# Kernel tuning notes

Measured on AMD Instinct MI355X. Metric: run time of the kernel, lower is better.

The kernel has to match this reference:

```python
import jax, jax.numpy as jnp
import numpy as np

INP = 256
OUP = 256
FGROUP = 16
CGROUP = 8
K = 3
STRIDE = 1
PAD = K // 2
B, H, W = 16, 64, 64
O1 = OUP * INP * K * K // CGROUP  # 73728, glgf output channels


def setup_inputs() -> dict:
    key = jax.random.key(0)
    ks = jax.random.split(key, 11)
    s = 0.1  # keep sigmoid pre-activations in a sane range
    return {
        "x": jax.random.normal(ks[0], (B, INP, H, W), jnp.float32),
        # GLGF generating the dynamic conv weights (oup*inp*k*k//cgroup outputs)
        "g1_fc1_l": jax.random.normal(ks[1], (INP, INP // FGROUP), jnp.float32) * s,
        "g1_fc1_g1": jax.random.normal(ks[2], (FGROUP, INP // FGROUP), jnp.float32) * s,
        "g1_fc1_g2": jax.random.normal(ks[3], (INP, FGROUP), jnp.float32) * s,
        "g1_fc2_l": jax.random.normal(ks[4], (O1,), jnp.float32) * s,
        "g1_fc2_g": jax.random.normal(ks[5], (INP,), jnp.float32) * s,
        # GLGF generating the per-channel output gate c (oup outputs)
        "g2_fc1_l": jax.random.normal(ks[6], (INP, INP // FGROUP), jnp.float32) * s,
        "g2_fc1_g1": jax.random.normal(ks[7], (FGROUP, INP // FGROUP), jnp.float32) * s,
        "g2_fc1_g2": jax.random.normal(ks[8], (INP, FGROUP), jnp.float32) * s,
        "g2_fc2_l": jax.random.normal(ks[9], (OUP,), jnp.float32) * s,
        "g2_fc2_g": jax.random.normal(ks[10], (INP,), jnp.float32) * s,
    }


def glgf(g, w1l, w1g1, w1g2, w2l, w2g):
    """GLGF applied to a [B, inp] gap vector (all convs are 1x1 -> grouped linears)."""
    b, inp = g.shape
    gp = inp // FGROUP
    gg = g.reshape(b, FGROUP, gp)
    # wn_fc1_l: grouped (fgroup) inp->inp; weight [inp, inp//fgroup]
    local = jnp.einsum('bgi,goi->bgo', gg, w1l.reshape(FGROUP, gp, gp)).reshape(b, inp)
    # wn_fc1_g2(wn_fc1_g1(x)): inp->fgroup (grouped) then fgroup->inp (dense)
    glob = jnp.einsum('bgi,gi->bg', gg, w1g1) @ w1g2.T  # [b, inp]
    h = jax.nn.sigmoid(local + glob)
    # wn_fc2_l: groups=inp, inp->O; weight [O] (1 input channel per output)
    O = w2l.shape[0]
    local2 = (h[:, :, None] * w2l.reshape(inp, O // inp)).reshape(b, O)
    # wn_fc2_g: dense inp->1, broadcast-added
    glob2 = h @ w2g  # [b]
    return local2 + glob2[:, None]


def reference(x, g1_fc1_l, g1_fc1_g1, g1_fc1_g2, g1_fc2_l, g1_fc2_g,
              g2_fc1_l, g2_fc1_g1, g2_fc1_g2, g2_fc2_l, g2_fc2_g):
    b = x.shape[0]
    gap = x.mean(axis=(2, 3))  # adaptive_avg_pool2d to 1x1 -> [b, inp]
    # generate per-sample grouped conv weights: [b, oup, inp//cgroup, k, k]
    xw = glgf(gap, g1_fc1_l, g1_fc1_g1, g1_fc1_g2, g1_fc2_l, g1_fc2_g)
    w = xw.reshape(b, OUP, INP // CGROUP, K, K)
    # torch's groups=b*cgroup batch-trick == per-sample conv with groups=cgroup
    def conv_one(xi, wi):
        return jax.lax.conv_general_dilated(
            xi[None], wi, (STRIDE, STRIDE), [(PAD, PAD), (PAD, PAD)],
            feature_group_count=CGROUP,
            dimension_numbers=('NCHW', 'OIHW', 'NCHW'))[0]
    y = jax.vmap(conv_one)(x, w)  # [b, oup, H, W]
    # per-sample, per-channel gate
    c = glgf(gap, g2_fc1_l, g2_fc1_g1, g2_fc1_g2, g2_fc2_l, g2_fc2_g)  # [b, oup]
    return y * c[:, :, None, None]
```

## Files before the change

kernel.cpp:

```cpp
#include <hip/hip_runtime.h>
#include <cstddef>
#include <cstdint>

typedef __attribute__((ext_vector_type(8))) short bf16x8;
typedef __attribute__((ext_vector_type(4))) unsigned short ushort4v;
typedef __attribute__((ext_vector_type(8))) unsigned short ushort8v;
typedef __attribute__((ext_vector_type(16))) float f32x16;

__device__ __forceinline__ unsigned short f2bf(float f) {
  union { float f; unsigned u; } v; v.f = f;
  unsigned r = v.u + 0x7FFFu + ((v.u >> 16) & 1u);
  return (unsigned short)(r >> 16);
}

__device__ __forceinline__ void gload16(const void* g, void* l) {
  __builtin_amdgcn_global_load_lds(
      (const __attribute__((address_space(1))) void*)(unsigned long long)(uintptr_t)g,
      (__attribute__((address_space(3))) void*)(unsigned)(uintptr_t)l, 16, 0, 0);
}

#define PADC 132
__global__ __launch_bounds__(256) void prep_kernel(
    const float* __restrict__ x, unsigned short* __restrict__ xt,
    float* __restrict__ partials) {
  __shared__ unsigned short cm[32 * PADC];
  __shared__ float sred[32][32];
  const int bid = blockIdx.x;
  const int wkr = ((bid & 7) << 9) | (bid >> 3);
  const int yp = wkr & 31, g = (wkr >> 5) & 7, b = wkr >> 8;
  const int y0 = yp * 2;
  const int tid = threadIdx.x;
  const float* xg = x + (size_t)(b * 256 + g * 32) * 4096;

  float csum[4];
#pragma unroll
  for (int j = 0; j < 4; ++j) {
    const int idx = tid + 256 * j;
    const int ic = idx >> 5;
    const int r = idx & 31;
    const int ry = r >> 4, gx4 = (r & 15) * 4;
    const float4 v = *reinterpret_cast<const float4*>(
        xg + (size_t)ic * 4096 + (y0 + ry) * 64 + gx4);
    csum[j] = v.x + v.y + v.z + v.w;
    ushort4v s;
    s[0] = f2bf(v.x); s[1] = f2bf(v.y); s[2] = f2bf(v.z); s[3] = f2bf(v.w);
    *reinterpret_cast<ushort4v*>(&cm[ic * PADC + ry * 64 + gx4]) = s;
  }
#pragma unroll
  for (int j = 0; j < 4; ++j) {
    const int ic = (tid >> 5) + 8 * j;
    sred[ic][tid & 31] = csum[j];
  }
  __syncthreads();

  if (tid < 32) {
    float s = 0.f;
#pragma unroll
    for (int i = 0; i < 32; ++i) s += sred[tid][i];
    partials[(size_t)(b * 256 + g * 32 + tid) * 32 + yp] = s;
  }

  const size_t xtb = (size_t)(b * 8 + g) * (66 * 66 * 32);
#pragma unroll
  for (int jj = 0; jj < 2; ++jj) {
    const int o = tid + 256 * jj;
    const int px = o >> 2, icq = o & 3;
    const int ry = px >> 6, gx = px & 63;
    ushort8v t;
#pragma unroll
    for (int c2 = 0; c2 < 8; ++c2) t[c2] = cm[(icq * 8 + c2) * PADC + px];
    *reinterpret_cast<ushort8v*>(
        &xt[xtb + ((size_t)(y0 + ry + 1) * 66 + (gx + 1)) * 32 + icq * 8]) = t;
  }

  const ushort8v z = {0, 0, 0, 0, 0, 0, 0, 0};
  if (tid < 16) {
    const int rr = tid >> 3;
    const int side = (tid >> 2) & 1;
    const int icq = tid & 3;
    const int col = side * 65;
    *reinterpret_cast<ushort8v*>(
        &xt[xtb + ((size_t)(y0 + rr + 1) * 66 + col) * 32 + icq * 8]) = z;
  }
  if (yp == 0 || yp == 31) {
    const int row = (yp == 0) ? 0 : 65;
    for (int o = tid; o < 66 * 4; o += 256) {
      const int col = o >> 2, icq = o & 3;
      *reinterpret_cast<ushort8v*>(
          &xt[xtb + ((size_t)row * 66 + col) * 32 + icq * 8]) = z;
    }
  }
}

__global__ __launch_bounds__(256) void glgf_pack(
    const float* __restrict__ partials,
    const float* __restrict__ w1l, const float* __restrict__ w1g1,
    const float* __restrict__ w1g2, const float* __restrict__ w2l,
    const float* __restrict__ w2g,
    const float* __restrict__ v1l, const float* __restrict__ v1g1,
    const float* __restrict__ v1g2, const float* __restrict__ v2l,
    const float* __restrict__ v2g,
    unsigned short* __restrict__ wpack) {
  __shared__ float gapL[256];
  __shared__ float t1L[16];
  __shared__ float h1L[256];
  __shared__ float red[256];
  __shared__ float cLs[32];
  const int bid = blockIdx.x;
  const int bg = ((bid & 7) << 4) | (bid >> 3);
  const int g = bg & 7, b = bg >> 3;
  const int c = threadIdx.x;
  {
    float s = 0.f;
    const float* pp = partials + (size_t)(b * 256 + c) * 32;
#pragma unroll
    for (int i = 0; i < 32; ++i) s += pp[i];
    gapL[c] = s * (1.f / 4096.f);
  }
  __syncthreads();

  const int gbase = c & ~15;
  float local1 = 0.f;
#pragma unroll
  for (int i = 0; i < 16; ++i) local1 += gapL[gbase + i] * w1l[c * 16 + i];
  if (c < 16) {
    float t = 0.f;
#pragma unroll
    for (int i = 0; i < 16; ++i) t += gapL[c * 16 + i] * w1g1[c * 16 + i];
    t1L[c] = t;
  }
  __syncthreads();
  float glob1 = 0.f;
#pragma unroll
  for (int gg = 0; gg < 16; ++gg) glob1 += t1L[gg] * w1g2[c * 16 + gg];
  const float h1 = 1.f / (1.f + expf(-(local1 + glob1)));
  h1L[c] = h1;
  red[c] = h1 * w2g[c];
  __syncthreads();
  for (int s = 128; s > 0; s >>= 1) {
    if (c < s) red[c] += red[c + s];
    __syncthreads();
  }
  const float glob2 = red[0];

  float local2 = 0.f;
#pragma unroll
  for (int i = 0; i < 16; ++i) local2 += gapL[gbase + i] * v1l[c * 16 + i];
  if (c < 16) {
    float t = 0.f;
#pragma unroll
    for (int i = 0; i < 16; ++i) t += gapL[c * 16 + i] * v1g1[c * 16 + i];
    t1L[c] = t;
  }
  __syncthreads();
  float glob1b = 0.f;
#pragma unroll
  for (int gg = 0; gg < 16; ++gg) glob1b += t1L[gg] * v1g2[c * 16 + gg];
  const float h2 = 1.f / (1.f + expf(-(local2 + glob1b)));
  red[c] = h2 * v2g[c];
  __syncthreads();
  for (int s = 128; s > 0; s >>= 1) {
    if (c < s) red[c] += red[c + s];
    __syncthreads();
  }
  if (c < 32) {
    const int o = g * 32 + c;
    float l = 0.f;
#pragma unroll
    for (int i = 0; i < 16; ++i) l += gapL[(o & ~15) + i] * v1l[o * 16 + i];
    float gl = 0.f;
#pragma unroll
    for (int gg = 0; gg < 16; ++gg) gl += t1L[gg] * v1g2[o * 16 + gg];
    const float h2o = 1.f / (1.f + expf(-(l + gl)));
    cLs[c] = h2o * v2l[o] + red[0];
  }
  __syncthreads();

  unsigned short* wpo = wpack + (size_t)bg * 9216;
#pragma unroll 4
  for (int it = 0; it < 36; ++it) {
    const int idx = it * 256 + c;
    const int kk = idx >> 9;
    const int rem = idx & 511;
    const int l = rem >> 3, e = rem & 7;
    const int oc = l & 31, hi = l >> 5;
    const int ic = ((kk & 1) << 4) + hi * 8 + e;
    const int sp = kk >> 1;
    const int o = (g << 5) + oc;
    const float wv = h1L[o] * w2l[o * 288 + ic * 9 + sp] + glob2;
    wpo[idx] = f2bf(wv * cLs[oc]);
  }
}

__global__ __launch_bounds__(512, 4) void conv_kernel(
    const unsigned short* __restrict__ wpack,
    const unsigned short* __restrict__ xt, float* __restrict__ out) {
  __shared__ __align__(16) unsigned short wpl[9216];
  __shared__ __align__(16) unsigned short btile[21120];

  const int bid = blockIdx.x;
  const int wkr = ((bid & 7) << 7) | (bid >> 3);
  const int yq = wkr & 7;
  const int bg = wkr >> 3;
  const int g = bg & 7, b = bg >> 3;
  const int tid = threadIdx.x;
  const int lane = tid & 63, wave = tid >> 6;
  const int n = lane & 31, hi = lane >> 5;

  const char* xbase = (const char*)xt + (size_t)bg * 278784;
  const int y0 = yq * 8;

#pragma unroll
  for (int i = 0; i < 6; ++i) {
    const int li = i * 512 + tid;
    if (li < 2640) {
      const int r = li / 264, rem = li - r * 264;
      const int cqs = rem / 66, px = rem % 66;
      const int cq = cqs ^ (px & 3);
      gload16(xbase + (y0 + r) * 4224 + px * 64 + cq * 16,
              (char*)btile + i * 8192 + wave * 1024);
    }
  }

  {
    const uint4* src = reinterpret_cast<const uint4*>(wpack + (size_t)bg * 9216);
    uint4* dst = reinterpret_cast<uint4*>(wpl);
#pragma unroll
    for (int i = 0; i < 3; ++i) {
      const int li = i * 512 + tid;
      if (li < 1152) dst[li] = src[li];
    }
  }

  asm volatile("s_waitcnt vmcnt(0) lgkmcnt(0)\n\ts_barrier" ::: "memory");
  __builtin_amdgcn_sched_barrier(0);

  f32x16 acc0, acc1;
#pragma unroll
  for (int i = 0; i < 16; ++i) { acc0[i] = 0.f; acc1[i] = 0.f; }

  __builtin_amdgcn_s_setprio(1);
#pragma unroll
  for (int kk = 0; kk < 18; ++kk) {
    const int sp = kk >> 1;
    const int ky = sp / 3, kx = sp % 3;
    const int cq = ((kk & 1) << 1) + hi;
    const int pxA = n + kx;
    const int pxB = 32 + n + kx;
    const bf16x8 af =
        *reinterpret_cast<const bf16x8*>(&wpl[kk * 512 + lane * 8]);
    const bf16x8 bf0 = *reinterpret_cast<const bf16x8*>(
        &btile[((((wave + ky) << 2) + (cq ^ (pxA & 3))) * 66 + pxA) * 8]);
    const bf16x8 bf1 = *reinterpret_cast<const bf16x8*>(
        &btile[((((wave + ky) << 2) + (cq ^ (pxB & 3))) * 66 + pxB) * 8]);
    acc0 = __builtin_amdgcn_mfma_f32_32x32x16_bf16(af, bf0, acc0, 0, 0, 0);
    acc1 = __builtin_amdgcn_mfma_f32_32x32x16_bf16(af, bf1, acc1, 0, 0, 0);
  }
  __builtin_amdgcn_s_setprio(0);

  const int y = y0 + wave;
  float* ob = out + (size_t)(b * 256 + g * 32) * 4096 + y * 64 + n +
              (size_t)(hi << 2) * 4096;
#pragma unroll
  for (int r = 0; r < 16; ++r) {
    const int row = (r & 3) + ((r >> 2) << 3);
    ob[(size_t)row * 4096] = acc0[r];
    ob[(size_t)row * 4096 + 32] = acc1[r];
  }
}

extern "C" void kernel_launch(void* const* d_in, const int* in_sizes, int n_in,
                              void* d_out, int out_size, void* d_ws,
                              size_t ws_size, hipStream_t stream) {
  const float* x    = (const float*)d_in[0];
  const float* w1l  = (const float*)d_in[1];
  const float* w1g1 = (const float*)d_in[2];
  const float* w1g2 = (const float*)d_in[3];
  const float* w2l  = (const float*)d_in[4];
  const float* w2g  = (const float*)d_in[5];
  const float* v1l  = (const float*)d_in[6];
  const float* v1g1 = (const float*)d_in[7];
  const float* v1g2 = (const float*)d_in[8];
  const float* v2l  = (const float*)d_in[9];
  const float* v2g  = (const float*)d_in[10];
  float* out = (float*)d_out;

  unsigned short* xt = (unsigned short*)d_ws;
  float* partials = (float*)(xt + 17842176);
  unsigned short* wpack = (unsigned short*)(partials + 131072);

  prep_kernel<<<4096, 256, 0, stream>>>(x, xt, partials);
  glgf_pack<<<128, 256, 0, stream>>>(partials, w1l, w1g1, w1g2, w2l, w2g,
                                     v1l, v1g1, v1g2, v2l, v2g, wpack);
  conv_kernel<<<1024, 512, 0, stream>>>(wpack, xt, out);
}
```

Baseline: 52.58 us.

## Fuse bf16 transpose/padding into conv kernel, drop intermediate xt buffer

Removes the prep kernel that wrote a padded channel-last bf16 copy of x to workspace. A lean GAP reduction kernel now computes the pooled vector, and the conv kernel reads fp32 x directly, converts it to bf16 and writes the swizzled LDS tile with zero halos. This avoids writing and re-reading the roughly 35 MB intermediate. In exchange, the conv blocks re-read halo rows of x, issue strided scalar global loads (one per channel per lane), and give up the async global-to-LDS loads.

```diff
diff --git a/kernel.cpp b/kernel.cpp
--- a/kernel.cpp
+++ b/kernel.cpp
@@ -3,7 +3,6 @@
 #include <cstdint>
 
 typedef __attribute__((ext_vector_type(8))) short bf16x8;
-typedef __attribute__((ext_vector_type(4))) unsigned short ushort4v;
 typedef __attribute__((ext_vector_type(8))) unsigned short ushort8v;
 typedef __attribute__((ext_vector_type(16))) float f32x16;
 
@@ -13,87 +12,27 @@
   return (unsigned short)(r >> 16);
 }
 
-__device__ __forceinline__ void gload16(const void* g, void* l) {
-  __builtin_amdgcn_global_load_lds(
-      (const __attribute__((address_space(1))) void*)(unsigned long long)(uintptr_t)g,
-      (__attribute__((address_space(3))) void*)(unsigned)(uintptr_t)l, 16, 0, 0);
-}
-
-#define PADC 132
-__global__ __launch_bounds__(256) void prep_kernel(
-    const float* __restrict__ x, unsigned short* __restrict__ xt,
-    float* __restrict__ partials) {
-  __shared__ unsigned short cm[32 * PADC];
-  __shared__ float sred[32][32];
+__global__ __launch_bounds__(256) void gap_kernel(const float* __restrict__ x,
+                                                  float* __restrict__ gap) {
   const int bid = blockIdx.x;
-  const int wkr = ((bid & 7) << 9) | (bid >> 3);
-  const int yp = wkr & 31, g = (wkr >> 5) & 7, b = wkr >> 8;
-  const int y0 = yp * 2;
-  const int tid = threadIdx.x;
-  const float* xg = x + (size_t)(b * 256 + g * 32) * 4096;
-
-  float csum[4];
+  const float* p = x + (size_t)bid * 4096;
+  const int t = threadIdx.x;
+  float s = 0.f;
 #pragma unroll
   for (int j = 0; j < 4; ++j) {
-    const int idx = tid + 256 * j;
-    const int ic = idx >> 5;
-    const int r = idx & 31;
-    const int ry = r >> 4, gx4 = (r & 15) * 4;
-    const float4 v = *reinterpret_cast<const float4*>(
-        xg + (size_t)ic * 4096 + (y0 + ry) * 64 + gx4);
-    csum[j] = v.x + v.y + v.z + v.w;
-    ushort4v s;
-    s[0] = f2bf(v.x); s[1] = f2bf(v.y); s[2] = f2bf(v.z); s[3] = f2bf(v.w);
-    *reinterpret_cast<ushort4v*>(&cm[ic * PADC + ry * 64 + gx4]) = s;
-  }
-#pragma unroll
-  for (int j = 0; j < 4; ++j) {
-    const int ic = (tid >> 5) + 8 * j;
-    sred[ic][tid & 31] = csum[j];
-  }
-  __syncthreads();
-
-  if (tid < 32) {
-    float s = 0.f;
-#pragma unroll
-    for (int i = 0; i < 32; ++i) s += sred[tid][i];
-    partials[(size_t)(b * 256 + g * 32 + tid) * 32 + yp] = s;
-  }
-
-  const size_t xtb = (size_t)(b * 8 + g) * (66 * 66 * 32);
-#pragma unroll
-  for (int jj = 0; jj < 2; ++jj) {
-    const int o = tid + 256 * jj;
-    const int px = o >> 2, icq = o & 3;
-    const int ry = px >> 6, gx = px & 63;
-    ushort8v t;
-#pragma unroll
-    for (int c2 = 0; c2 < 8; ++c2) t[c2] = cm[(icq * 8 + c2) * PADC + px];
-    *reinterpret_cast<ushort8v*>(
-        &xt[xtb + ((size_t)(y0 + ry + 1) * 66 + (gx + 1)) * 32 + icq * 8]) = t;
-  }
-
-  const ushort8v z = {0, 0, 0, 0, 0, 0, 0, 0};
-  if (tid < 16) {
-    const int rr = tid >> 3;
-    const int side = (tid >> 2) & 1;
-    const int icq = tid & 3;
-    const int col = side * 65;
-    *reinterpret_cast<ushort8v*>(
-        &xt[xtb + ((size_t)(y0 + rr + 1) * 66 + col) * 32 + icq * 8]) = z;
-  }
-  if (yp == 0 || yp == 31) {
-    const int row = (yp == 0) ? 0 : 65;
-    for (int o = tid; o < 66 * 4; o += 256) {
-      const int col = o >> 2, icq = o & 3;
-      *reinterpret_cast<ushort8v*>(
-          &xt[xtb + ((size_t)row * 66 + col) * 32 + icq * 8]) = z;
-    }
-  }
+    const float4 v = *reinterpret_cast<const float4*>(p + j * 1024 + t * 4);
+    s += v.x + v.y + v.z + v.w;
+  }
+#pragma unroll
+  for (int off = 32; off > 0; off >>= 1) s += __shfl_down(s, off, 64);
+  __shared__ float ws[4];
+  if ((t & 63) == 0) ws[t >> 6] = s;
+  __syncthreads();
+  if (t == 0) gap[bid] = (ws[0] + ws[1] + ws[2] + ws[3]) * (1.f / 4096.f);
 }
 
 __global__ __launch_bounds__(256) void glgf_pack(
-    const float* __restrict__ partials,
+    const float* __restrict__ gap,
     const float* __restrict__ w1l, const float* __restrict__ w1g1,
     const float* __restrict__ w1g2, const float* __restrict__ w2l,
     const float* __restrict__ w2g,
@@ -110,13 +49,7 @@
   const int bg = ((bid & 7) << 4) | (bid >> 3);
   const int g = bg & 7, b = bg >> 3;
   const int c = threadIdx.x;
-  {
-    float s = 0.f;
-    const float* pp = partials + (size_t)(b * 256 + c) * 32;
-#pragma unroll
-    for (int i = 0; i < 32; ++i) s += pp[i];
-    gapL[c] = s * (1.f / 4096.f);
-  }
+  gapL[c] = gap[b * 256 + c];
   __syncthreads();
 
   const int gbase = c & ~15;
@@ -193,8 +126,8 @@
 }
 
 __global__ __launch_bounds__(512, 4) void conv_kernel(
-    const unsigned short* __restrict__ wpack,
-    const unsigned short* __restrict__ xt, float* __restrict__ out) {
+    const float* __restrict__ x, const unsigned short* __restrict__ wpack,
+    float* __restrict__ out) {
   __shared__ __align__(16) unsigned short wpl[9216];
   __shared__ __align__(16) unsigned short btile[21120];
 
@@ -206,21 +139,7 @@
   const int tid = threadIdx.x;
   const int lane = tid & 63, wave = tid >> 6;
   const int n = lane & 31, hi = lane >> 5;
-
-  const char* xbase = (const char*)xt + (size_t)bg * 278784;
   const int y0 = yq * 8;
-
-#pragma unroll
-  for (int i = 0; i < 6; ++i) {
-    const int li = i * 512 + tid;
-    if (li < 2640) {
-      const int r = li / 264, rem = li - r * 264;
-      const int cqs = rem / 66, px = rem % 66;
-      const int cq = cqs ^ (px & 3);
-      gload16(xbase + (y0 + r) * 4224 + px * 64 + cq * 16,
-              (char*)btile + i * 8192 + wave * 1024);
-    }
-  }
 
   {
     const uint4* src = reinterpret_cast<const uint4*>(wpack + (size_t)bg * 9216);
@@ -232,8 +151,30 @@
     }
   }
 
-  asm volatile("s_waitcnt vmcnt(0) lgkmcnt(0)\n\ts_barrier" ::: "memory");
-  __builtin_amdgcn_sched_barrier(0);
+  const float* xg = x + (size_t)(b * 256 + g * 32) * 4096;
+#pragma unroll
+  for (int i = 0; i < 5; ++i) {
+    const int t = wave * 5 + i;
+    const int r = t >> 2, icq = t & 3;
+    const int y = y0 - 1 + r;
+    const bool ok = (y >= 0) && (y < 64);
+    ushort8v cell;
+#pragma unroll
+    for (int j = 0; j < 8; ++j) {
+      const float v = ok ? xg[(size_t)(icq * 8 + j) * 4096 + y * 64 + lane] : 0.f;
+      cell[j] = f2bf(v);
+    }
+    const int px = lane + 1;
+    *reinterpret_cast<ushort8v*>(
+        &btile[((r * 4 + (icq ^ (px & 3))) * 66 + px) * 8]) = cell;
+  }
+  if (tid < 80) {
+    const int r = tid >> 3, c8 = tid & 7;
+    const int cq = c8 & 3, px = (c8 >> 2) ? 65 : 0;
+    const ushort8v z = {0, 0, 0, 0, 0, 0, 0, 0};
+    *reinterpret_cast<ushort8v*>(&btile[((r * 4 + cq) * 66 + px) * 8]) = z;
+  }
+  __syncthreads();
 
   f32x16 acc0, acc1;
 #pragma unroll
@@ -285,12 +226,11 @@
   const float* v2g  = (const float*)d_in[10];
   float* out = (float*)d_out;
 
-  unsigned short* xt = (unsigned short*)d_ws;
-  float* partials = (float*)(xt + 17842176);
-  unsigned short* wpack = (unsigned short*)(partials + 131072);
-
-  prep_kernel<<<4096, 256, 0, stream>>>(x, xt, partials);
-  glgf_pack<<<128, 256, 0, stream>>>(partials, w1l, w1g1, w1g2, w2l, w2g,
+  float* gap = (float*)d_ws;
+  unsigned short* wpack = (unsigned short*)(gap + 4096);
+
+  gap_kernel<<<4096, 256, 0, stream>>>(x, gap);
+  glgf_pack<<<128, 256, 0, stream>>>(gap, w1l, w1g1, w1g2, w2l, w2g,
                                      v1l, v1g1, v1g2, v2l, v2g, wpack);
-  conv_kernel<<<1024, 512, 0, stream>>>(wpack, xt, out);
-}
+  conv_kernel<<<1024, 512, 0, stream>>>(x, wpack, out);
+}
```

Result: faster. 50.39 us (-4.2%).
